# Performance work log

Hardware: AMD Instinct MI355X
Metric: run time of the kernel (lower is better)

Reference implementation:

```python
import jax, jax.numpy as jnp
import numpy as np

# Module hyperparams (from init_kwargs)
B, C, F, K, H, W = 8, 32, 32, 3, 32, 32
Q = K * K          # kernel positions
PAD = K // 2       # 'same' padding (output spatial == input spatial)
# groups = in_channels (num_groups=None default) -> step = 1, weight axis = F*Q*C


def setup_inputs() -> dict:
    key = jax.random.key(0)
    k1, k2, k3 = jax.random.split(key, 3)
    x = jax.random.normal(k1, (B, C, H, W), dtype=jnp.float32)
    # learned per-weight rational coefficients: one rational per (f, kernel_pos, channel)
    nums = jax.random.normal(k2, (F * Q * C, 6), dtype=jnp.float32) * 0.1
    denoms = jax.random.normal(k3, (F * Q * C, 4), dtype=jnp.float32) * 0.1
    return {"x": x, "nums": nums, "denoms": denoms}


def reference(x, nums, denoms):
    # per-weight Pade rational activation over conv windows, scatter-accumulated
    # into output channels:
    #   out[b,f,y,x] = sum_{q in KxK, c} P_{f,q,c}(w) / (1 + |D_{f,q,c}(w)|),
    #   w = zero-padded input at window position q, channel c.
    a = nums.reshape(F, Q, C, 6)    # numerator coeffs, powers 0..5
    b = denoms.reshape(F, Q, C, 4)  # denominator coeffs, powers 1..4

    xp = jnp.pad(x, ((0, 0), (0, 0), (PAD, PAD), (PAD, PAD)))
    # gather K*K shifted views: [B, C, Q, H, W]
    win = jnp.stack([xp[:, :, i:i + H, j:j + W]
                     for i in range(K) for j in range(K)], axis=2)

    # powers w^0..w^5: [B, C, Q, 6, H, W]
    w1 = win
    w2 = w1 * w1
    w3 = w2 * w1
    w4 = w2 * w2
    w5 = w4 * w1
    pows = jnp.stack([jnp.ones_like(w1), w1, w2, w3, w4, w5], axis=3)

    # numerator P and denominator D, per (f, q, c): [B, F, Q, C, H, W]
    num = jnp.einsum('bcqphw,fqcp->bfqchw', pows, a)
    den = 1.0 + jnp.abs(jnp.einsum('bcqphw,fqcp->bfqchw', pows[:, :, :, 1:5], b))

    # accumulate over kernel positions and channels -> [B, F, H, W]
    return jnp.sum(num / den, axis=(2, 3))
```

## Files before the change

### kernel.cpp

```cpp
#include <hip/hip_runtime.h>
#include <math.h>

#define NB 8
#define NC 32
#define NF 32
#define NH 32
#define NW 32
#define NQ 9
#define TS 34
#define TILE_N (TS * TS)

__global__ __launch_bounds__(256) void ka_conv_rational_kernel(
    const float* __restrict__ x,
    const float* __restrict__ nums,
    const float* __restrict__ dens,
    float* __restrict__ out)
{
    __shared__ float tile[2][TILE_N];

    const int t    = threadIdx.x;
    const int bid  = blockIdx.x;
    const int half = bid & 1;
    const int bf   = bid >> 1;
    const int f    = bf & (NF - 1);
    const int bb   = bf >> 5;
    const int xx   = t & 31;
    const int y0   = half * 16 + ((t >> 5) << 1);

    int  soff[5];
    bool svalid[5];
#pragma unroll
    for (int i = 0; i < 5; ++i) {
        int idx = t + i * 256;
        int ry  = idx / TS;
        int rx  = idx - ry * TS;
        bool ok = (idx < TILE_N) && (ry >= 1) && (ry <= NH) && (rx >= 1) && (rx <= NW);
        svalid[i] = ok;
        soff[i]   = ok ? ((ry - 1) * NW + (rx - 1)) : 0;
    }

    const float* __restrict__ xb    = x    + (size_t)bb * NC * NH * NW;
    const float* __restrict__ abase = nums + (size_t)f * NQ * NC * 6;
    const float* __restrict__ bbase = dens + (size_t)f * NQ * NC * 4;

    float st[5];
#pragma unroll
    for (int i = 0; i < 5; ++i)
        st[i] = xb[soff[i]];

    float acc0 = 0.f, acc1 = 0.f;

    for (int c = 0; c < NC; ++c) {
        float* tl = tile[c & 1];

#pragma unroll
        for (int i = 0; i < 5; ++i) {
            int idx = t + i * 256;
            if (idx < TILE_N)
                tl[idx] = svalid[i] ? st[i] : 0.f;
        }
        if (c + 1 < NC) {
            const float* xc = xb + (size_t)(c + 1) * NH * NW;
#pragma unroll
            for (int i = 0; i < 5; ++i)
                st[i] = xc[soff[i]];
        }
        __syncthreads();

        float n[4][3];
#pragma unroll
        for (int dy = 0; dy < 4; ++dy)
#pragma unroll
            for (int dx = 0; dx < 3; ++dx)
                n[dy][dx] = tl[(y0 + dy) * TS + (xx + dx)];

#pragma unroll
        for (int q = 0; q < NQ; ++q) {
            const float* ap = abase + (size_t)(q * NC + c) * 6;
            const float* bp = bbase + (size_t)(q * NC + c) * 4;
            const float a0 = ap[0], a1 = ap[1], a2 = ap[2],
                        a3 = ap[3], a4 = ap[4], a5 = ap[5];
            const float d0 = bp[0], d1 = bp[1], d2 = bp[2], d3 = bp[3];
            const int qi = q / 3, qj = q - qi * 3;

            {
                const float w  = n[qi][qj];
                float nu = fmaf(fmaf(fmaf(fmaf(fmaf(a5, w, a4), w, a3), w, a2), w, a1), w, a0);
                float dp = fmaf(fmaf(fmaf(d3, w, d2), w, d1), w, d0) * w;
                float de = 1.0f + fabsf(dp);
                acc0 = fmaf(nu, __builtin_amdgcn_rcpf(de), acc0);
            }
            {
                const float w  = n[qi + 1][qj];
                float nu = fmaf(fmaf(fmaf(fmaf(fmaf(a5, w, a4), w, a3), w, a2), w, a1), w, a0);
                float dp = fmaf(fmaf(fmaf(d3, w, d2), w, d1), w, d0) * w;
                float de = 1.0f + fabsf(dp);
                acc1 = fmaf(nu, __builtin_amdgcn_rcpf(de), acc1);
            }
        }
    }

    float* op = out + ((size_t)bf * NH + y0) * NW + xx;
    op[0]  = acc0;
    op[NW] = acc1;
}

extern "C" void kernel_launch(void* const* d_in, const int* in_sizes, int n_in,
                              void* d_out, int out_size, void* d_ws, size_t ws_size,
                              hipStream_t stream) {
    const float* x    = (const float*)d_in[0];
    const float* nums = (const float*)d_in[1];
    const float* dens = (const float*)d_in[2];
    float* out = (float*)d_out;

    dim3 grid(NB * NF * 2);
    dim3 block(256);
    ka_conv_rational_kernel<<<grid, block, 0, stream>>>(x, nums, dens, out);
}
```

Before: 96.41 us.

## Split channel reduction across blocks with atomics and packed float2 math

Splits the 32-channel reduction four ways across blocks, so the grid grows fourfold and each block stages a half-height tile of 18 rows. Partial sums are combined into the output with atomic adds after a memset. The rational evaluation is also rewritten on 2-wide float vectors so packed FMA instructions can be used, and the launch bounds now request higher occupancy. The cost is the atomic traffic, an extra memset launch, and a nondeterministic summation order.

```diff
diff --git a/kernel.cpp b/kernel.cpp
--- a/kernel.cpp
+++ b/kernel.cpp
@@ -7,10 +7,16 @@
 #define NH 32
 #define NW 32
 #define NQ 9
+#define CSPLIT 4
+#define CPB (NC / CSPLIT)
+#define TROWS 18
 #define TS 34
-#define TILE_N (TS * TS)
+#define TILE_N (TROWS * TS)
 
-__global__ __launch_bounds__(256) void ka_conv_rational_kernel(
+typedef float f2 __attribute__((ext_vector_type(2)));
+__device__ __forceinline__ f2 sp(float v) { return (f2){v, v}; }
+
+__global__ __launch_bounds__(256, 8) void ka_conv_rational_kernel(
     const float* __restrict__ x,
     const float* __restrict__ nums,
     const float* __restrict__ dens,
@@ -20,49 +26,54 @@
 
     const int t    = threadIdx.x;
     const int bid  = blockIdx.x;
-    const int half = bid & 1;
-    const int bf   = bid >> 1;
+    const int cs   = bid & (CSPLIT - 1);
+    const int half = (bid >> 2) & 1;
+    const int bf   = bid >> 3;
     const int f    = bf & (NF - 1);
     const int bb   = bf >> 5;
     const int xx   = t & 31;
-    const int y0   = half * 16 + ((t >> 5) << 1);
+    const int ty   = t >> 5;
+    const int c0   = cs * CPB;
 
-    int  soff[5];
-    bool svalid[5];
+    int  soff[3];
+    bool svalid[3];
 #pragma unroll
-    for (int i = 0; i < 5; ++i) {
+    for (int i = 0; i < 3; ++i) {
         int idx = t + i * 256;
         int ry  = idx / TS;
         int rx  = idx - ry * TS;
-        bool ok = (idx < TILE_N) && (ry >= 1) && (ry <= NH) && (rx >= 1) && (rx <= NW);
+        int gy  = half * 16 + ry - 1;
+        int gx  = rx - 1;
+        bool ok = (idx < TILE_N) && (gy >= 0) && (gy < NH) && (gx >= 0) && (gx < NW);
         svalid[i] = ok;
-        soff[i]   = ok ? ((ry - 1) * NW + (rx - 1)) : 0;
+        soff[i]   = ok ? (gy * NW + gx) : 0;
     }
 
-    const float* __restrict__ xb    = x    + (size_t)bb * NC * NH * NW;
+    const float* __restrict__ xb    = x    + ((size_t)bb * NC + c0) * NH * NW;
     const float* __restrict__ abase = nums + (size_t)f * NQ * NC * 6;
     const float* __restrict__ bbase = dens + (size_t)f * NQ * NC * 4;
 
-    float st[5];
+    float st[3];
 #pragma unroll
-    for (int i = 0; i < 5; ++i)
+    for (int i = 0; i < 3; ++i)
         st[i] = xb[soff[i]];
 
-    float acc0 = 0.f, acc1 = 0.f;
+    f2 acc = {0.f, 0.f};
 
-    for (int c = 0; c < NC; ++c) {
-        float* tl = tile[c & 1];
+    for (int ci = 0; ci < CPB; ++ci) {
+        const int c = c0 + ci;
+        float* tl = tile[ci & 1];
 
 #pragma unroll
-        for (int i = 0; i < 5; ++i) {
+        for (int i = 0; i < 3; ++i) {
             int idx = t + i * 256;
             if (idx < TILE_N)
                 tl[idx] = svalid[i] ? st[i] : 0.f;
         }
-        if (c + 1 < NC) {
-            const float* xc = xb + (size_t)(c + 1) * NH * NW;
+        if (ci + 1 < CPB) {
+            const float* xc = xb + (size_t)(ci + 1) * NH * NW;
 #pragma unroll
-            for (int i = 0; i < 5; ++i)
+            for (int i = 0; i < 3; ++i)
                 st[i] = xc[soff[i]];
         }
         __syncthreads();
@@ -72,7 +83,7 @@
         for (int dy = 0; dy < 4; ++dy)
 #pragma unroll
             for (int dx = 0; dx < 3; ++dx)
-                n[dy][dx] = tl[(y0 + dy) * TS + (xx + dx)];
+                n[dy][dx] = tl[(ty * 2 + dy) * TS + (xx + dx)];
 
 #pragma unroll
         for (int q = 0; q < NQ; ++q) {
@@ -83,26 +94,26 @@
             const float d0 = bp[0], d1 = bp[1], d2 = bp[2], d3 = bp[3];
             const int qi = q / 3, qj = q - qi * 3;
 
-            {
-                const float w  = n[qi][qj];
-                float nu = fmaf(fmaf(fmaf(fmaf(fmaf(a5, w, a4), w, a3), w, a2), w, a1), w, a0);
-                float dp = fmaf(fmaf(fmaf(d3, w, d2), w, d1), w, d0) * w;
-                float de = 1.0f + fabsf(dp);
-                acc0 = fmaf(nu, __builtin_amdgcn_rcpf(de), acc0);
-            }
-            {
-                const float w  = n[qi + 1][qj];
-                float nu = fmaf(fmaf(fmaf(fmaf(fmaf(a5, w, a4), w, a3), w, a2), w, a1), w, a0);
-                float dp = fmaf(fmaf(fmaf(d3, w, d2), w, d1), w, d0) * w;
-                float de = 1.0f + fabsf(dp);
-                acc1 = fmaf(nu, __builtin_amdgcn_rcpf(de), acc1);
-            }
+            f2 w = {n[qi][qj], n[qi + 1][qj]};
+            f2 nu = __builtin_elementwise_fma(sp(a5), w, sp(a4));
+            nu = __builtin_elementwise_fma(nu, w, sp(a3));
+            nu = __builtin_elementwise_fma(nu, w, sp(a2));
+            nu = __builtin_elementwise_fma(nu, w, sp(a1));
+            nu = __builtin_elementwise_fma(nu, w, sp(a0));
+            f2 dp = __builtin_elementwise_fma(sp(d3), w, sp(d2));
+            dp = __builtin_elementwise_fma(dp, w, sp(d1));
+            dp = __builtin_elementwise_fma(dp, w, sp(d0));
+            dp = dp * w;
+            f2 de = 1.0f + __builtin_elementwise_abs(dp);
+            f2 r  = {__builtin_amdgcn_rcpf(de.x), __builtin_amdgcn_rcpf(de.y)};
+            acc = __builtin_elementwise_fma(nu, r, acc);
         }
     }
 
+    const int y0 = half * 16 + ty * 2;
     float* op = out + ((size_t)bf * NH + y0) * NW + xx;
-    op[0]  = acc0;
-    op[NW] = acc1;
+    unsafeAtomicAdd(op, acc.x);
+    unsafeAtomicAdd(op + NW, acc.y);
 }
 
 extern "C" void kernel_launch(void* const* d_in, const int* in_sizes, int n_in,
@@ -113,7 +124,9 @@
     const float* dens = (const float*)d_in[2];
     float* out = (float*)d_out;
 
-    dim3 grid(NB * NF * 2);
+    hipMemsetAsync(d_out, 0, (size_t)out_size * sizeof(float), stream);
+
+    dim3 grid(NB * NF * 2 * CSPLIT);
     dim3 block(256);
     ka_conv_rational_kernel<<<grid, block, 0, stream>>>(x, nums, dens, out);
 }
```

New measurement: 82.04 us. -14.9%, faster.
